# Kernel optimization log

Hardware: AMD Instinct MI355X
Metric: run time of the kernel (lower is better)

Reference implementation:

```python
import jax, jax.numpy as jnp
import numpy as np

N = 50000          # num nodes
E = 800000         # num edges (before self loops)
IN_C = 128
HID = 256          # heads * head_dim
HEADS = 4
HEAD_DIM = HID // HEADS
OUT_C = 64
NEG_SLOPE = 0.2    # PyG GATConv default leaky_relu slope
BN_EPS = 1e-5


def _gat_conv(x, src, dst, W, att_src, att_dst, bias, concat):
    """PyG-style GATConv (with self loops already appended to src/dst).
    x: [N, in_c]; W: [in_c, H*C]; att_src/att_dst: [H, C]; bias: [H*C] or [C]."""
    H, C = att_src.shape
    h = (x @ W).reshape(-1, H, C)                               # [N, H, C]
    a_src = jnp.einsum('nhc,hc->nh', h, att_src)                # [N, H]
    a_dst = jnp.einsum('nhc,hc->nh', h, att_dst)                # [N, H]
    e = jax.nn.leaky_relu(a_src[src] + a_dst[dst], NEG_SLOPE)   # [Et, H]
    # segment softmax over destination nodes (numerically stable)
    m = jax.ops.segment_max(e, dst, num_segments=N)             # [N, H]
    m = jnp.where(jnp.isfinite(m), m, 0.0)
    ex = jnp.exp(e - m[dst])
    denom = jax.ops.segment_sum(ex, dst, num_segments=N)        # [N, H]
    alpha = ex / (denom[dst] + 1e-16)                           # [Et, H]
    msg = alpha[:, :, None] * h[src]                            # [Et, H, C]
    out = jax.ops.segment_sum(msg, dst, num_segments=N)         # [N, H, C]
    out = out.reshape(N, H * C) if concat else out.mean(axis=1)
    return out + bias


def _bn_eval(x, gamma, beta, mean, var):
    return (x - mean) * jax.lax.rsqrt(var + BN_EPS) * gamma + beta


def setup_inputs() -> dict:
    key = jax.random.key(0)
    ks = jax.random.split(key, 16)
    x = jax.random.normal(ks[0], (N, IN_C), dtype=jnp.float32)
    edge_index = jax.random.randint(ks[1], (2, E), 0, N, dtype=jnp.int64)

    def lin(k, fan_in, fan_out):
        s = (1.0 / np.sqrt(fan_in)).astype(np.float32)
        return jax.random.normal(k, (fan_in, fan_out), dtype=jnp.float32) * s

    def att(k, h, c):
        return jax.random.normal(k, (h, c), dtype=jnp.float32) * 0.1

    return {
        'x': x, 'edge_index': edge_index,
        'W0': lin(ks[2], IN_C, HID), 'as0': att(ks[3], HEADS, HEAD_DIM), 'ad0': att(ks[4], HEADS, HEAD_DIM), 'b0': jnp.zeros((HID,), jnp.float32),
        'bn0_g': jnp.ones((HID,), jnp.float32), 'bn0_b': jnp.zeros((HID,), jnp.float32), 'bn0_m': jnp.zeros((HID,), jnp.float32), 'bn0_v': jnp.ones((HID,), jnp.float32),
        'W1': lin(ks[5], HID, HID), 'as1': att(ks[6], HEADS, HEAD_DIM), 'ad1': att(ks[7], HEADS, HEAD_DIM), 'b1': jnp.zeros((HID,), jnp.float32),
        'bn1_g': jnp.ones((HID,), jnp.float32), 'bn1_b': jnp.zeros((HID,), jnp.float32), 'bn1_m': jnp.zeros((HID,), jnp.float32), 'bn1_v': jnp.ones((HID,), jnp.float32),
        'W2': lin(ks[8], HID, OUT_C), 'as2': att(ks[9], 1, OUT_C), 'ad2': att(ks[10], 1, OUT_C), 'b2': jnp.zeros((OUT_C,), jnp.float32),
    }


def reference(x, edge_index, W0, as0, ad0, b0, bn0_g, bn0_b, bn0_m, bn0_v,
              W1, as1, ad1, b1, bn1_g, bn1_b, bn1_m, bn1_v,
              W2, as2, ad2, b2):
    loop = jnp.arange(N, dtype=edge_index.dtype)
    src = jnp.concatenate([edge_index[0], loop])   # PyG add_self_loops=True
    dst = jnp.concatenate([edge_index[1], loop])

    h = _gat_conv(x, src, dst, W0, as0, ad0, b0, concat=True)
    h = jax.nn.elu(_bn_eval(h, bn0_g, bn0_b, bn0_m, bn0_v))   # dropout: eval -> identity
    h = _gat_conv(h, src, dst, W1, as1, ad1, b1, concat=True)
    h = jax.nn.elu(_bn_eval(h, bn1_g, bn1_b, bn1_m, bn1_v))
    out = _gat_conv(h, src, dst, W2, as2, ad2, b2, concat=False)  # heads=1, mean
    return out
```

## Files before the change

kernel.cpp:

```cpp
#include <hip/hip_runtime.h>

#define NN   50000
#define EE   800000
#define ET   850000
#define INC  128
#define HID  256
#define OUTC 64
#define NEG  0.2f
#define BNEPS 1e-5f

typedef __bf16 bf16x8 __attribute__((ext_vector_type(8)));
typedef float  f32x4  __attribute__((ext_vector_type(4)));

static __device__ __forceinline__ float b2f(unsigned short u) {
    return __uint_as_float(((unsigned)u) << 16);
}
static __device__ __forceinline__ float blo(unsigned u) {
    return __uint_as_float(u << 16);
}
static __device__ __forceinline__ float bhi(unsigned u) {
    return __uint_as_float(u & 0xFFFF0000u);
}
static __device__ __forceinline__ unsigned short f2b(float f) {
    unsigned u = __float_as_uint(f);
    unsigned r = u + 0x7FFFu + ((u >> 16) & 1u);
    return (unsigned short)(r >> 16);
}
static __device__ __forceinline__ float leaky(float x) {
    return x > 0.f ? x : NEG * x;
}
static __device__ __forceinline__ float ew(float e) {
    return __expf(fminf(e, 80.f));
}

__global__ void k_init(const int* __restrict__ ei, const unsigned* __restrict__ xw,
                       int* __restrict__ cnt, int* __restrict__ flagW, int* __restrict__ flagB,
                       int nbZ) {
    __shared__ int cs[4];
    int b = blockIdx.x, t = threadIdx.x;
    if (b < nbZ) {
        int i = b * 256 + t;
        if (i < NN) cnt[i] = 0;
    } else if (b == nbZ) {
        int c = 0;
        for (int k = 0; k < 16; k++) {
            int i = t + 256 * k;
            if (ei[2 * i + 1] != 0) c = 1;
        }
        for (int o = 1; o < 64; o <<= 1) c |= __shfl_xor(c, o);
        if ((t & 63) == 0) cs[t >> 6] = c;
        __syncthreads();
        if (t == 0) *flagW = cs[0] | cs[1] | cs[2] | cs[3];
    } else {
        int c = 0;
        for (int i = t; i < 4096; i += 256) {
            unsigned v = (xw[i] >> 8) & 0x7F;
            if (v >= 50 && v <= 67) c++;
        }
        for (int o = 1; o < 64; o <<= 1) c += __shfl_xor(c, o);
        if ((t & 63) == 0) cs[t >> 6] = c;
        __syncthreads();
        if (t == 0) *flagB = (cs[0] + cs[1] + cs[2] + cs[3] > 2048) ? 1 : 0;
    }
}

__global__ void k_prep(const void* as0, const void* ad0, const void* b0, const void* g0,
                       const void* be0, const void* m0, const void* v0,
                       const void* as1, const void* ad1, const void* b1, const void* g1,
                       const void* be1, const void* m1, const void* v1,
                       const void* as2, const void* ad2, const void* b2,
                       const void* W0, const void* W1, const void* W2,
                       unsigned short* __restrict__ WT0, unsigned short* __restrict__ WT1,
                       unsigned short* __restrict__ WT2,
                       const void* __restrict__ x, unsigned short* __restrict__ xb,
                       float* __restrict__ pp, const int* __restrict__ flagB) {
    int b = blockIdx.x, t = threadIdx.x;
    bool bf = (*flagB != 0);
    auto cv = [&](const void* s, int i) -> float {
        return bf ? b2f(((const unsigned short*)s)[i]) : ((const float*)s)[i];
    };
    if (b < 14) {
        float v;
        switch (b) {
            case 0:  v = cv(as0, t); break;
            case 1:  v = cv(ad0, t); break;
            case 2:  v = cv(b0, t);  break;
            case 3:  v = cv(g0, t);  break;
            case 4:  v = cv(be0, t); break;
            case 5:  v = cv(m0, t);  break;
            case 6:  v = cv(v0, t);  break;
            case 7:  v = cv(as1, t); break;
            case 8:  v = cv(ad1, t); break;
            case 9:  v = cv(b1, t);  break;
            case 10: v = cv(g1, t);  break;
            case 11: v = cv(be1, t); break;
            case 12: v = cv(m1, t);  break;
            default: v = cv(v1, t);  break;
        }
        pp[b * 256 + t] = v;
    } else if (b == 14) {
        if (t < 192) {
            int arr = t >> 6, j = t & 63;
            float v = (arr == 0) ? cv(as2, j) : (arr == 1) ? cv(ad2, j) : cv(b2, j);
            pp[14 * 256 + arr * 64 + j] = v;
        }
    } else if (b < 15 + 128) {
        int i = (b - 15) * 256 + t;
        int k = i >> 8, n = i & 255;
        WT0[n * INC + k] = bf ? ((const unsigned short*)W0)[i] : f2b(((const float*)W0)[i]);
    } else if (b < 15 + 128 + 256) {
        int i = (b - 143) * 256 + t;
        int k = i >> 8, n = i & 255;
        WT1[n * HID + k] = bf ? ((const unsigned short*)W1)[i] : f2b(((const float*)W1)[i]);
    } else if (b < 15 + 128 + 256 + 64) {
        int i = (b - 399) * 256 + t;
        int k = i >> 6, n = i & 63;
        WT2[n * HID + k] = bf ? ((const unsigned short*)W2)[i] : f2b(((const float*)W2)[i]);
    } else {
        if (bf) return;
        int i = (b - 463) * 256 + t;
        if (i < NN * INC)
            xb[i] = f2b(((const float*)x)[i]);
    }
}

__global__ void k_hist(const int* __restrict__ ei, const int* __restrict__ flagW,
                       int* __restrict__ cnt) {
    int i = blockIdx.x * 256 + threadIdx.x;
    if (i >= ET) return;
    bool w32 = (*flagW != 0);
    int d = (i < EE) ? (w32 ? ei[EE + i] : ei[2 * (EE + i)]) : (i - EE);
    atomicAdd(&cnt[d], 1);
}

static __device__ __forceinline__ int block_scan_incl(int v, int t, int* ws) {
    int lane = t & 63, w = t >> 6;
    int x = v;
    for (int o = 1; o < 64; o <<= 1) {
        int y = __shfl_up(x, o);
        if (lane >= o) x += y;
    }
    if (lane == 63) ws[w] = x;
    __syncthreads();
    if (t == 0) {
        int s = 0;
        for (int k = 0; k < 4; k++) { int tmp = ws[k]; ws[k] = s; s += tmp; }
    }
    __syncthreads();
    return x + ws[w];
}

__global__ void k_scan_a(const int* __restrict__ cnt, int* __restrict__ rowptr, int* __restrict__ bsum) {
    __shared__ int ws[4];
    int t = threadIdx.x, b = blockIdx.x;
    int i = b * 256 + t;
    int v = (i < NN) ? cnt[i] : 0;
    int incl = block_scan_incl(v, t, ws);
    if (i < NN) rowptr[i] = incl - v;
    if (t == 255) bsum[b] = incl;
}

__global__ void k_scan_b(int* __restrict__ bsum, int nb) {
    __shared__ int ws[4];
    int t = threadIdx.x;
    int v = (t < nb) ? bsum[t] : 0;
    int incl = block_scan_incl(v, t, ws);
    if (t < nb) bsum[t] = incl - v;
}

__global__ void k_scan_c(int* __restrict__ rowptr, const int* __restrict__ bsum, int* __restrict__ cursor) {
    int t = threadIdx.x, b = blockIdx.x;
    int i = b * 256 + t;
    if (i < NN) {
        int r = rowptr[i] + bsum[b];
        rowptr[i] = r;
        cursor[i] = r;
    }
    if (i == 0) rowptr[NN] = ET;
}

__global__ void k_scatter(const int* __restrict__ ei, const int* __restrict__ flagW,
                          int* __restrict__ cursor, int* __restrict__ esrc) {
    int i = blockIdx.x * 256 + threadIdx.x;
    if (i >= ET) {
        if (i < ET + 64) esrc[i] = 0;
        return;
    }
    bool w32 = (*flagW != 0);
    int s, d;
    if (i < EE) {
        if (w32) { s = ei[i];     d = ei[EE + i]; }
        else     { s = ei[2 * i]; d = ei[2 * (EE + i)]; }
    } else {
        s = d = i - EE;
    }
    int p = atomicAdd(&cursor[d], 1);
    esrc[p] = s;
}

template<int NC, int NH>
__global__ __launch_bounds__(256) void k_gemm(const unsigned short* __restrict__ Amain,
                                              const void* __restrict__ Aalt,
                                              const int* __restrict__ flagB,
                                              const unsigned short* __restrict__ WT,
                                              unsigned short* __restrict__ H,
                                              float* __restrict__ asrc, float* __restrict__ adst,
                                              const float* __restrict__ asv, const float* __restrict__ adv,
                                              int M, int K) {
    __shared__ __align__(16) unsigned short As[128 * 40];
    __shared__ __align__(16) unsigned short Bs[64 * 40];
    const unsigned short* A = (*flagB) ? (const unsigned short*)Aalt : Amain;
    int t = threadIdx.x;
    int bm = blockIdx.x, bn = blockIdx.y;
    int lane = t & 63, wave = t >> 6;
    int m16 = lane & 15, quad = lane >> 4;

    f32x4 acc[2][4];
    for (int a = 0; a < 2; a++) for (int b = 0; b < 4; b++) acc[a][b] = (f32x4){0.f, 0.f, 0.f, 0.f};

    int arow = t >> 1, ahalf = t & 1;
    int brow = t >> 2, bq = t & 3;
    long gArow = (long)bm * 128 + arow;

    for (int k0 = 0; k0 < K; k0 += 32) {
        uint4 av0 = {0u, 0u, 0u, 0u}, av1 = {0u, 0u, 0u, 0u};
        if (gArow < M) {
            const unsigned short* ap = A + gArow * (size_t)K + k0 + ahalf * 16;
            av0 = *(const uint4*)(ap);
            av1 = *(const uint4*)(ap + 8);
        }
        uint4 bv = *(const uint4*)(WT + ((size_t)bn * 64 + brow) * K + k0 + bq * 8);
        *(uint4*)&As[arow * 40 + ahalf * 16]     = av0;
        *(uint4*)&As[arow * 40 + ahalf * 16 + 8] = av1;
        *(uint4*)&Bs[brow * 40 + bq * 8]         = bv;
        __syncthreads();
        int wrow = wave * 32;
        bf16x8 af[2], bf[4];
        for (int mt = 0; mt < 2; mt++)
            af[mt] = *(const bf16x8*)&As[(wrow + mt * 16 + m16) * 40 + quad * 8];
        for (int nt = 0; nt < 4; nt++)
            bf[nt] = *(const bf16x8*)&Bs[(nt * 16 + m16) * 40 + quad * 8];
        for (int mt = 0; mt < 2; mt++)
            for (int nt = 0; nt < 4; nt++)
                acc[mt][nt] = __builtin_amdgcn_mfma_f32_16x16x32_bf16(af[mt], bf[nt], acc[mt][nt], 0, 0, 0);
        __syncthreads();
    }

    float asc[4], adc[4];
    for (int nt = 0; nt < 4; nt++) {
        int col = bn * 64 + nt * 16 + m16;
        asc[nt] = asv[col];
        adc[nt] = adv[col];
    }
    for (int mt = 0; mt < 2; mt++) {
        int gR0 = bm * 128 + wave * 32 + mt * 16 + quad * 4;
        for (int r = 0; r < 4; r++) {
            int gR = gR0 + r;
            float ps = 0.f, pd = 0.f;
            for (int nt = 0; nt < 4; nt++) {
                float v = acc[mt][nt][r];
                ps += v * asc[nt];
                pd += v * adc[nt];
            }
            for (int o = 1; o < 16; o <<= 1) { ps += __shfl_xor(ps, o); pd += __shfl_xor(pd, o); }
            if (m16 == 0 && gR < M) {
                asrc[(size_t)gR * NH + bn] = ps;
                adst[(size_t)gR * NH + bn] = pd;
            }
            if (gR < M) {
                for (int nt = 0; nt < 4; nt++) {
                    int gC = bn * 64 + nt * 16 + m16;
                    H[(size_t)gR * NC + gC] = f2b(acc[mt][nt][r]);
                }
            }
        }
    }
}

#define LOADG(pre, d, e0n) \
    uint2 pre##0 = {0, 0}, pre##1 = {0, 0}, pre##2 = {0, 0}, pre##3 = {0, 0}; \
    if (d) { \
        int s0_ = esrc[(e0n)], s1_ = esrc[(e0n) + 1], s2_ = esrc[(e0n) + 2], s3_ = esrc[(e0n) + 3]; \
        pre##0 = *(const uint2*)(h + (size_t)s0_ * HID + lc); \
        pre##1 = *(const uint2*)(h + (size_t)s1_ * HID + lc); \
        pre##2 = *(const uint2*)(h + (size_t)s2_ * HID + lc); \
        pre##3 = *(const uint2*)(h + (size_t)s3_ * HID + lc); \
    }
#define FMAG(pre, d, wreg, A0, A1, A2, A3, j) \
    if (d) { \
        float w0_ = __shfl(wreg, wsel + (j)),     w1_ = __shfl(wreg, wsel + (j) + 1); \
        float w2_ = __shfl(wreg, wsel + (j) + 2), w3_ = __shfl(wreg, wsel + (j) + 3); \
        A0 += w0_ * blo((pre##0).x) + w1_ * blo((pre##1).x) + w2_ * blo((pre##2).x) + w3_ * blo((pre##3).x); \
        A1 += w0_ * bhi((pre##0).x) + w1_ * bhi((pre##1).x) + w2_ * bhi((pre##2).x) + w3_ * bhi((pre##3).x); \
        A2 += w0_ * blo((pre##0).y) + w1_ * blo((pre##1).y) + w2_ * blo((pre##2).y) + w3_ * blo((pre##3).y); \
        A3 += w0_ * bhi((pre##0).y) + w1_ * bhi((pre##1).y) + w2_ * bhi((pre##2).y) + w3_ * bhi((pre##3).y); \
    }

__global__ __launch_bounds__(256, 4) void k_agg4(const unsigned short* __restrict__ h,
                       const float* __restrict__ asrc, const float* __restrict__ adst,
                       const int* __restrict__ rowptr, const int* __restrict__ esrc,
                       const float* __restrict__ bias,
                       const float* __restrict__ bng, const float* __restrict__ bnb,
                       const float* __restrict__ bnm, const float* __restrict__ bnv,
                       unsigned short* __restrict__ act) {
    int t = threadIdx.x;
    int wave = t >> 6, lane = t & 63;
    int nodeA = blockIdx.x * 8 + wave * 2;
    if (nodeA >= NN) return;
    int nodeB = nodeA + 1;
    bool hasB = (nodeB < NN);

    int hd = lane >> 4, li = lane & 15;
    int wsel = lane & 48;
    const size_t lc = (size_t)lane * 4;

    int e0A = __builtin_amdgcn_readfirstlane(rowptr[nodeA]);
    int e1A = __builtin_amdgcn_readfirstlane(rowptr[nodeA + 1]);
    int degA = e1A - e0A;
    int e0B = e1A, degB = 0;
    if (hasB) degB = __builtin_amdgcn_readfirstlane(rowptr[nodeB + 1]) - e1A;

    float adhA = adst[(size_t)nodeA * 4 + hd];
    float adhB = hasB ? adst[(size_t)nodeB * 4 + hd] : 0.f;

    float waccA = 0.f, waccB = 0.f;
    float aA0 = 0.f, aA1 = 0.f, aA2 = 0.f, aA3 = 0.f;
    float aB0 = 0.f, aB1 = 0.f, aB2 = 0.f, aB3 = 0.f;

    int nA = min(16, degA), nB = min(16, degB);
    float eA = 0.f, eB = 0.f;
    if (li < nA) { int s = esrc[e0A + li]; eA = asrc[(size_t)s * 4 + hd]; }
    if (li < nB) { int s = esrc[e0B + li]; eB = asrc[(size_t)s * 4 + hd]; }

    int degM = max(degA, degB);
    for (int c = 0; c < degM; c += 16) {
        float wA = (li < nA) ? ew(leaky(eA + adhA)) : 0.f;
        float wB = (li < nB) ? ew(leaky(eB + adhB)) : 0.f;
        waccA += wA; waccB += wB;
        int nA2 = min(16, degA - (c + 16));
        int nB2 = min(16, degB - (c + 16));
        eA = 0.f; eB = 0.f;
        if (li < nA2) { int s = esrc[e0A + c + 16 + li]; eA = asrc[(size_t)s * 4 + hd]; }
        if (li < nB2) { int s = esrc[e0B + c + 16 + li]; eB = asrc[(size_t)s * 4 + hd]; }
        bool dA0 = 0 < nA, dA1 = 4 < nA, dA2 = 8 < nA, dA3 = 12 < nA;
        bool dB0 = 0 < nB, dB1 = 4 < nB, dB2 = 8 < nB, dB3 = 12 < nB;
        LOADG(gA0, dA0, e0A + c)
        LOADG(gA1, dA1, e0A + c + 4)
        LOADG(gA2, dA2, e0A + c + 8)
        LOADG(gA3, dA3, e0A + c + 12)
        LOADG(gB0, dB0, e0B + c)
        LOADG(gB1, dB1, e0B + c + 4)
        LOADG(gB2, dB2, e0B + c + 8)
        LOADG(gB3, dB3, e0B + c + 12)
        FMAG(gA0, dA0, wA, aA0, aA1, aA2, aA3, 0)
        FMAG(gA1, dA1, wA, aA0, aA1, aA2, aA3, 4)
        FMAG(gA2, dA2, wA, aA0, aA1, aA2, aA3, 8)
        FMAG(gA3, dA3, wA, aA0, aA1, aA2, aA3, 12)
        FMAG(gB0, dB0, wB, aB0, aB1, aB2, aB3, 0)
        FMAG(gB1, dB1, wB, aB0, aB1, aB2, aB3, 4)
        FMAG(gB2, dB2, wB, aB0, aB1, aB2, aB3, 8)
        FMAG(gB3, dB3, wB, aB0, aB1, aB2, aB3, 12)
        nA = nA2; nB = nB2;
    }
    waccA += __shfl_xor(waccA, 1); waccA += __shfl_xor(waccA, 2);
    waccA += __shfl_xor(waccA, 4); waccA += __shfl_xor(waccA, 8);
    waccB += __shfl_xor(waccB, 1); waccB += __shfl_xor(waccB, 2);
    waccB += __shfl_xor(waccB, 4); waccB += __shfl_xor(waccB, 8);
    float invA = 1.f / (waccA + 1e-16f);
    float invB = 1.f / (waccB + 1e-16f);

    int c0 = lane * 4;
    float4 bi = *(const float4*)(bias + c0);
    float4 bm_ = *(const float4*)(bnm + c0);
    float4 bv_ = *(const float4*)(bnv + c0);
    float4 bg_ = *(const float4*)(bng + c0);
    float4 bb_ = *(const float4*)(bnb + c0);
    float sc[4], sh[4];
    {
        const float* bvp = (const float*)&bv_;
        const float* bgp = (const float*)&bg_;
        const float* bmp = (const float*)&bm_;
        const float* bbp = (const float*)&bb_;
        const float* bip = (const float*)&bi;
        #pragma unroll
        for (int jj = 0; jj < 4; jj++) {
            float s_ = rsqrtf(bvp[jj] + BNEPS) * bgp[jj];
            sc[jj] = s_;
            sh[jj] = bbp[jj] + (bip[jj] - bmp[jj]) * s_;
        }
    }
    {
        float o[4] = {aA0 * invA, aA1 * invA, aA2 * invA, aA3 * invA};
        unsigned short res[4];
        #pragma unroll
        for (int jj = 0; jj < 4; jj++) {
            float val = o[jj] * sc[jj] + sh[jj];
            val = val > 0.f ? val : expm1f(val);
            res[jj] = f2b(val);
        }
        *(ushort4*)(act + (size_t)nodeA * HID + c0) = *(ushort4*)res;
    }
    if (hasB) {
        float o[4] = {aB0 * invB, aB1 * invB, aB2 * invB, aB3 * invB};
        unsigned short res[4];
        #pragma unroll
        for (int jj = 0; jj < 4; jj++) {
            float val = o[jj] * sc[jj] + sh[jj];
            val = val > 0.f ? val : expm1f(val);
            res[jj] = f2b(val);
        }
        *(ushort4*)(act + (size_t)nodeB * HID + c0) = *(ushort4*)res;
    }
}

__global__ void k_agg1(const unsigned short* __restrict__ h,
                       const float* __restrict__ asrc, const float* __restrict__ adst,
                       const int* __restrict__ rowptr, const int* __restrict__ esrc,
                       const float* __restrict__ bias,
                       void* __restrict__ outp, const int* __restrict__ flagB) {
    int t = threadIdx.x;
    int wave = t >> 6, lane = t & 63;
    int nodeA = blockIdx.x * 8 + wave * 2;
    if (nodeA >= NN) return;
    int nodeB = nodeA + 1;
    bool hasB = (nodeB < NN);

    int e0A  = __builtin_amdgcn_readfirstlane(rowptr[nodeA]);
    int e1A  = __builtin_amdgcn_readfirstlane(rowptr[nodeA + 1]);
    int degA = e1A - e0A;
    int e0B  = e1A;
    int degB = hasB ? (__builtin_amdgcn_readfirstlane(rowptr[nodeB + 1]) - e1A) : 0;
    float adA = adst[nodeA];
    float adB = hasB ? adst[nodeB] : 0.f;

    float denA = 0.f, denB = 0.f, accA = 0.f, accB = 0.f;

    int nA = min(64, degA), nB = min(64, degB);
    float eA = 0.f, eB = 0.f;
    if (lane < nA) { int s = esrc[e0A + lane]; eA = asrc[s]; }
    if (lane < nB) { int s = esrc[e0B + lane]; eB = asrc[s]; }

    int degM = max(degA, degB);
    for (int c = 0; c < degM; c += 64) {
        float wA = (lane < nA) ? ew(leaky(eA + adA)) : 0.f;
        float wB = (lane < nB) ? ew(leaky(eB + adB)) : 0.f;
        denA += wA; denB += wB;
        int nA2 = min(64, degA - (c + 64));
        int nB2 = min(64, degB - (c + 64));
        eA = 0.f; eB = 0.f;
        if (lane < nA2) { int s = esrc[e0A + c + 64 + lane]; eA = asrc[s]; }
        if (lane < nB2) { int s = esrc[e0B + c + 64 + lane]; eB = asrc[s]; }
        int nM = max(nA, nB);
        for (int j = 0; j < nM; j += 4) {
            bool doA = j < nA, doB = j < nB;
            float w0A = 0.f, w1A = 0.f, w2A = 0.f, w3A = 0.f;
            float w0B = 0.f, w1B = 0.f, w2B = 0.f, w3B = 0.f;
            unsigned short hA0 = 0, hA1 = 0, hA2 = 0, hA3 = 0;
            unsigned short hB0 = 0, hB1 = 0, hB2 = 0, hB3 = 0;
            if (doA) {
                int s0 = esrc[e0A + c + j];     int s1 = esrc[e0A + c + j + 1];
                int s2 = esrc[e0A + c + j + 2]; int s3 = esrc[e0A + c + j + 3];
                w0A = __shfl(wA, j);     w1A = __shfl(wA, j + 1);
                w2A = __shfl(wA, j + 2); w3A = __shfl(wA, j + 3);
                hA0 = h[(size_t)s0 * OUTC + lane];
                hA1 = h[(size_t)s1 * OUTC + lane];
                hA2 = h[(size_t)s2 * OUTC + lane];
                hA3 = h[(size_t)s3 * OUTC + lane];
            }
            if (doB) {
                int s0 = esrc[e0B + c + j];     int s1 = esrc[e0B + c + j + 1];
                int s2 = esrc[e0B + c + j + 2]; int s3 = esrc[e0B + c + j + 3];
                w0B = __shfl(wB, j);     w1B = __shfl(wB, j + 1);
                w2B = __shfl(wB, j + 2); w3B = __shfl(wB, j + 3);
                hB0 = h[(size_t)s0 * OUTC + lane];
                hB1 = h[(size_t)s1 * OUTC + lane];
                hB2 = h[(size_t)s2 * OUTC + lane];
                hB3 = h[(size_t)s3 * OUTC + lane];
            }
            if (doA) accA += w0A * b2f(hA0) + w1A * b2f(hA1) + w2A * b2f(hA2) + w3A * b2f(hA3);
            if (doB) accB += w0B * b2f(hB0) + w1B * b2f(hB1) + w2B * b2f(hB2) + w3B * b2f(hB3);
        }
        nA = nA2; nB = nB2;
    }
    for (int o = 1; o < 64; o <<= 1) denA += __shfl_xor(denA, o);
    for (int o = 1; o < 64; o <<= 1) denB += __shfl_xor(denB, o);
    float valA = accA / (denA + 1e-16f) + bias[lane];
    float valB = accB / (denB + 1e-16f) + bias[lane];
    if (*flagB) {
        ((unsigned short*)outp)[(size_t)nodeA * OUTC + lane] = f2b(valA);
        if (hasB) ((unsigned short*)outp)[(size_t)nodeB * OUTC + lane] = f2b(valB);
    } else {
        ((float*)outp)[(size_t)nodeA * OUTC + lane] = valA;
        if (hasB) ((float*)outp)[(size_t)nodeB * OUTC + lane] = valB;
    }
}

extern "C" void kernel_launch(void* const* d_in, const int* in_sizes, int n_in,
                              void* d_out, int out_size, void* d_ws, size_t ws_size,
                              hipStream_t stream) {
    const void* x  = d_in[0];
    const int*  ei = (const int*)d_in[1];
    const void* W0 = d_in[2];
    const void* W1 = d_in[10];
    const void* W2 = d_in[18];

    char* ws = (char*)d_ws;
    size_t off = 0;
    auto alloc = [&](size_t n) { void* p = ws + off; off += (n + 255) & ~(size_t)255; return p; };

    unsigned short* xb  = (unsigned short*)alloc((size_t)NN * INC * 2);
    unsigned short* h   = (unsigned short*)alloc((size_t)NN * HID * 2);
    unsigned short* act = (unsigned short*)alloc((size_t)NN * HID * 2);
    unsigned short* WT0 = (unsigned short*)alloc((size_t)HID * INC * 2);
    unsigned short* WT1 = (unsigned short*)alloc((size_t)HID * HID * 2);
    unsigned short* WT2 = (unsigned short*)alloc((size_t)OUTC * HID * 2);
    float*          pp  = (float*)alloc((size_t)(14 * 256 + 3 * 64) * 4);
    float*  asrc   = (float*)alloc((size_t)NN * 4 * 4);
    float*  adst   = (float*)alloc((size_t)NN * 4 * 4);
    int*    cnt    = (int*)alloc((size_t)(NN + 2) * 4);
    int*    rowptr = (int*)alloc((size_t)(NN + 1) * 4);
    int*    cursor = (int*)alloc((size_t)NN * 4);
    int*    esrc   = (int*)alloc((size_t)(ET + 64) * 4);
    int*    bsum   = (int*)alloc(256 * 4);
    int*    flagW  = cnt + NN;
    int*    flagB  = cnt + NN + 1;

    float* P0 = pp;
    float* P1 = pp + 7 * 256;
    float* P2 = pp + 14 * 256;

    const int nbN = (NN + 255) / 256;
    const int nbE = (ET + 255) / 256;
    const int nbA4 = (NN + 7) / 8;
    const int nbA1 = (NN + 7) / 8;
    const int nbPrep = 463 + (NN * INC + 255) / 256;
    dim3 gemmGrid0((NN + 127) / 128, HID / 64);
    dim3 gemmGrid2((NN + 127) / 128, 1);

    k_init<<<nbN + 2, 256, 0, stream>>>(ei, (const unsigned*)x, cnt, flagW, flagB, nbN);
    k_hist<<<nbE, 256, 0, stream>>>(ei, flagW, cnt);
    k_scan_a<<<nbN, 256, 0, stream>>>(cnt, rowptr, bsum);
    k_scan_b<<<1, 256, 0, stream>>>(bsum, nbN);
    k_scan_c<<<nbN, 256, 0, stream>>>(rowptr, bsum, cursor);
    k_scatter<<<nbE, 256, 0, stream>>>(ei, flagW, cursor, esrc);

    k_prep<<<nbPrep, 256, 0, stream>>>(d_in[3], d_in[4], d_in[5], d_in[6], d_in[7], d_in[8], d_in[9],
                                       d_in[11], d_in[12], d_in[13], d_in[14], d_in[15], d_in[16], d_in[17],
                                       d_in[19], d_in[20], d_in[21],
                                       W0, W1, W2, WT0, WT1, WT2, x, xb, pp, flagB);

    k_gemm<HID, 4><<<gemmGrid0, 256, 0, stream>>>(xb, x, flagB, WT0, h, asrc, adst,
                                                  P0 + 0, P0 + 256, NN, INC);
    k_agg4<<<nbA4, 256, 0, stream>>>(h, asrc, adst, rowptr, esrc,
                                     P0 + 512, P0 + 768, P0 + 1024, P0 + 1280, P0 + 1536, act);

    k_gemm<HID, 4><<<gemmGrid0, 256, 0, stream>>>(act, act, flagB, WT1, h, asrc, adst,
                                                  P1 + 0, P1 + 256, NN, HID);
    k_agg4<<<nbA4, 256, 0, stream>>>(h, asrc, adst, rowptr, esrc,
                                     P1 + 512, P1 + 768, P1 + 1024, P1 + 1280, P1 + 1536, act);

    k_gemm<OUTC, 1><<<gemmGrid2, 256, 0, stream>>>(act, act, flagB, WT2, h, asrc, adst,
                                                   P2 + 0, P2 + 64, NN, HID);
    k_agg1<<<nbA1, 256, 0, stream>>>(h, asrc, adst, rowptr, esrc, P2 + 128, d_out, flagB);
}
```

Before: 446.4 us.

## Widen GEMM N-tile, restructure final aggregation, grid-stride x conversion

The GEMM is templated on the number of 64-column groups, so the hidden layers use 128-wide N tiles. Each A tile is then reused across two heads, which halves the grid's y dimension and the redundant A loads. The last aggregation kernel now assigns four nodes per wave, each on a 16-lane quarter that gathers 4 channels with 8-byte loads, in place of two nodes per wave with 2-byte per-lane loads. The x-to-bf16 prep becomes a grid-stride loop over a fixed 2048 blocks, and register pressure rises in the GEMM.

Result: faster. 434.7 us (-2.6%).

```diff
diff --git a/kernel.cpp b/kernel.cpp
--- a/kernel.cpp
+++ b/kernel.cpp
@@ -118,8 +118,7 @@
         WT2[n * HID + k] = bf ? ((const unsigned short*)W2)[i] : f2b(((const float*)W2)[i]);
     } else {
         if (bf) return;
-        int i = (b - 463) * 256 + t;
-        if (i < NN * INC)
+        for (int i = (b - 463) * 256 + t; i < NN * INC; i += 2048 * 256)
             xb[i] = f2b(((const float*)x)[i]);
     }
 }
@@ -198,7 +197,7 @@
     esrc[p] = s;
 }
 
-template<int NC, int NH>
+template<int NC, int NH, int NBN>
 __global__ __launch_bounds__(256) void k_gemm(const unsigned short* __restrict__ Amain,
                                               const void* __restrict__ Aalt,
                                               const int* __restrict__ flagB,
@@ -207,19 +206,22 @@
                                               float* __restrict__ asrc, float* __restrict__ adst,
                                               const float* __restrict__ asv, const float* __restrict__ adv,
                                               int M, int K) {
+    constexpr int BN = 64 * NBN;
     __shared__ __align__(16) unsigned short As[128 * 40];
-    __shared__ __align__(16) unsigned short Bs[64 * 40];
+    __shared__ __align__(16) unsigned short Bs[BN * 40];
     const unsigned short* A = (*flagB) ? (const unsigned short*)Aalt : Amain;
     int t = threadIdx.x;
-    int bm = blockIdx.x, bn = blockIdx.y;
+    int bm = blockIdx.x, bg = blockIdx.y;
     int lane = t & 63, wave = t >> 6;
     int m16 = lane & 15, quad = lane >> 4;
 
-    f32x4 acc[2][4];
-    for (int a = 0; a < 2; a++) for (int b = 0; b < 4; b++) acc[a][b] = (f32x4){0.f, 0.f, 0.f, 0.f};
+    f32x4 acc[2][4 * NBN];
+    #pragma unroll
+    for (int a = 0; a < 2; a++)
+        #pragma unroll
+        for (int b = 0; b < 4 * NBN; b++) acc[a][b] = (f32x4){0.f, 0.f, 0.f, 0.f};
 
     int arow = t >> 1, ahalf = t & 1;
-    int brow = t >> 2, bq = t & 3;
     long gArow = (long)bm * 128 + arow;
 
     for (int k0 = 0; k0 < K; k0 += 32) {
@@ -229,47 +231,70 @@
             av0 = *(const uint4*)(ap);
             av1 = *(const uint4*)(ap + 8);
         }
-        uint4 bv = *(const uint4*)(WT + ((size_t)bn * 64 + brow) * K + k0 + bq * 8);
-        *(uint4*)&As[arow * 40 + ahalf * 16]     = av0;
-        *(uint4*)&As[arow * 40 + ahalf * 16 + 8] = av1;
-        *(uint4*)&Bs[brow * 40 + bq * 8]         = bv;
+        if constexpr (NBN == 2) {
+            const unsigned short* bp = WT + ((size_t)bg * BN + arow) * K + k0 + ahalf * 16;
+            uint4 bv0 = *(const uint4*)(bp);
+            uint4 bv1 = *(const uint4*)(bp + 8);
+            *(uint4*)&As[arow * 40 + ahalf * 16]     = av0;
+            *(uint4*)&As[arow * 40 + ahalf * 16 + 8] = av1;
+            *(uint4*)&Bs[arow * 40 + ahalf * 16]     = bv0;
+            *(uint4*)&Bs[arow * 40 + ahalf * 16 + 8] = bv1;
+        } else {
+            int brow = t >> 2, bq = t & 3;
+            uint4 bv = *(const uint4*)(WT + ((size_t)bg * BN + brow) * K + k0 + bq * 8);
+            *(uint4*)&As[arow * 40 + ahalf * 16]     = av0;
+            *(uint4*)&As[arow * 40 + ahalf * 16 + 8] = av1;
+            *(uint4*)&Bs[brow * 40 + bq * 8]         = bv;
+        }
         __syncthreads();
         int wrow = wave * 32;
-        bf16x8 af[2], bf[4];
+        bf16x8 af[2], bf[4 * NBN];
+        #pragma unroll
         for (int mt = 0; mt < 2; mt++)
             af[mt] = *(const bf16x8*)&As[(wrow + mt * 16 + m16) * 40 + quad * 8];
-        for (int nt = 0; nt < 4; nt++)
+        #pragma unroll
+        for (int nt = 0; nt < 4 * NBN; nt++)
             bf[nt] = *(const bf16x8*)&Bs[(nt * 16 + m16) * 40 + quad * 8];
+        #pragma unroll
         for (int mt = 0; mt < 2; mt++)
-            for (int nt = 0; nt < 4; nt++)
+            #pragma unroll
+            for (int nt = 0; nt < 4 * NBN; nt++)
                 acc[mt][nt] = __builtin_amdgcn_mfma_f32_16x16x32_bf16(af[mt], bf[nt], acc[mt][nt], 0, 0, 0);
         __syncthreads();
     }
 
-    float asc[4], adc[4];
-    for (int nt = 0; nt < 4; nt++) {
-        int col = bn * 64 + nt * 16 + m16;
+    float asc[4 * NBN], adc[4 * NBN];
+    #pragma unroll
+    for (int nt = 0; nt < 4 * NBN; nt++) {
+        int col = bg * BN + nt * 16 + m16;
         asc[nt] = asv[col];
         adc[nt] = adv[col];
     }
+    #pragma unroll
     for (int mt = 0; mt < 2; mt++) {
         int gR0 = bm * 128 + wave * 32 + mt * 16 + quad * 4;
+        #pragma unroll
         for (int r = 0; r < 4; r++) {
             int gR = gR0 + r;
-            float ps = 0.f, pd = 0.f;
-            for (int nt = 0; nt < 4; nt++) {
-                float v = acc[mt][nt][r];
-                ps += v * asc[nt];
-                pd += v * adc[nt];
-            }
-            for (int o = 1; o < 16; o <<= 1) { ps += __shfl_xor(ps, o); pd += __shfl_xor(pd, o); }
-            if (m16 == 0 && gR < M) {
-                asrc[(size_t)gR * NH + bn] = ps;
-                adst[(size_t)gR * NH + bn] = pd;
+            #pragma unroll
+            for (int hh = 0; hh < NBN; hh++) {
+                float ps = 0.f, pd = 0.f;
+                #pragma unroll
+                for (int nt = hh * 4; nt < hh * 4 + 4; nt++) {
+                    float v = acc[mt][nt][r];
+                    ps += v * asc[nt];
+                    pd += v * adc[nt];
+                }
+                for (int o = 1; o < 16; o <<= 1) { ps += __shfl_xor(ps, o); pd += __shfl_xor(pd, o); }
+                if (m16 == 0 && gR < M) {
+                    asrc[(size_t)gR * NH + bg * NBN + hh] = ps;
+                    adst[(size_t)gR * NH + bg * NBN + hh] = pd;
+                }
             }
             if (gR < M) {
-                for (int nt = 0; nt < 4; nt++) {
-                    int gC = bn * 64 + nt * 16 + m16;
+                #pragma unroll
+                for (int nt = 0; nt < 4 * NBN; nt++) {
+                    int gC = bg * BN + nt * 16 + m16;
                     H[(size_t)gR * NC + gC] = f2b(acc[mt][nt][r]);
                 }
             }
@@ -420,78 +445,69 @@
                        void* __restrict__ outp, const int* __restrict__ flagB) {
     int t = threadIdx.x;
     int wave = t >> 6, lane = t & 63;
-    int nodeA = blockIdx.x * 8 + wave * 2;
-    if (nodeA >= NN) return;
-    int nodeB = nodeA + 1;
-    bool hasB = (nodeB < NN);
-
-    int e0A  = __builtin_amdgcn_readfirstlane(rowptr[nodeA]);
-    int e1A  = __builtin_amdgcn_readfirstlane(rowptr[nodeA + 1]);
-    int degA = e1A - e0A;
-    int e0B  = e1A;
-    int degB = hasB ? (__builtin_amdgcn_readfirstlane(rowptr[nodeB + 1]) - e1A) : 0;
-    float adA = adst[nodeA];
-    float adB = hasB ? adst[nodeB] : 0.f;
-
-    float denA = 0.f, denB = 0.f, accA = 0.f, accB = 0.f;
-
-    int nA = min(64, degA), nB = min(64, degB);
-    float eA = 0.f, eB = 0.f;
-    if (lane < nA) { int s = esrc[e0A + lane]; eA = asrc[s]; }
-    if (lane < nB) { int s = esrc[e0B + lane]; eB = asrc[s]; }
-
-    int degM = max(degA, degB);
-    for (int c = 0; c < degM; c += 64) {
-        float wA = (lane < nA) ? ew(leaky(eA + adA)) : 0.f;
-        float wB = (lane < nB) ? ew(leaky(eB + adB)) : 0.f;
-        denA += wA; denB += wB;
-        int nA2 = min(64, degA - (c + 64));
-        int nB2 = min(64, degB - (c + 64));
-        eA = 0.f; eB = 0.f;
-        if (lane < nA2) { int s = esrc[e0A + c + 64 + lane]; eA = asrc[s]; }
-        if (lane < nB2) { int s = esrc[e0B + c + 64 + lane]; eB = asrc[s]; }
-        int nM = max(nA, nB);
-        for (int j = 0; j < nM; j += 4) {
-            bool doA = j < nA, doB = j < nB;
-            float w0A = 0.f, w1A = 0.f, w2A = 0.f, w3A = 0.f;
-            float w0B = 0.f, w1B = 0.f, w2B = 0.f, w3B = 0.f;
-            unsigned short hA0 = 0, hA1 = 0, hA2 = 0, hA3 = 0;
-            unsigned short hB0 = 0, hB1 = 0, hB2 = 0, hB3 = 0;
-            if (doA) {
-                int s0 = esrc[e0A + c + j];     int s1 = esrc[e0A + c + j + 1];
-                int s2 = esrc[e0A + c + j + 2]; int s3 = esrc[e0A + c + j + 3];
-                w0A = __shfl(wA, j);     w1A = __shfl(wA, j + 1);
-                w2A = __shfl(wA, j + 2); w3A = __shfl(wA, j + 3);
-                hA0 = h[(size_t)s0 * OUTC + lane];
-                hA1 = h[(size_t)s1 * OUTC + lane];
-                hA2 = h[(size_t)s2 * OUTC + lane];
-                hA3 = h[(size_t)s3 * OUTC + lane];
+    int node0 = blockIdx.x * 16 + wave * 4;
+    int q = lane >> 4, lq = lane & 15;
+    int qs = lane & 48;
+    int node = node0 + q;
+    const size_t lc4 = (size_t)lq * 4;
+
+    int e0  = rowptr[node];
+    int deg = rowptr[node + 1] - e0;
+    float ad = adst[node];
+
+    float den = 0.f;
+    float a0 = 0.f, a1 = 0.f, a2 = 0.f, a3 = 0.f;
+
+    int n = min(16, deg);
+    int s = 0; float e = 0.f;
+    if (lq < n) { s = esrc[e0 + lq]; e = asrc[s]; }
+
+    int degM = deg;
+    degM = max(degM, __shfl_xor(degM, 16));
+    degM = max(degM, __shfl_xor(degM, 32));
+
+    for (int c = 0; c < degM; c += 16) {
+        float w = (lq < n) ? ew(leaky(e + ad)) : 0.f;
+        den += w;
+        int n2 = min(16, deg - (c + 16));
+        int sN = 0; float eN = 0.f;
+        if (lq < n2) { sN = esrc[e0 + c + 16 + lq]; eN = asrc[sN]; }
+        #pragma unroll
+        for (int g = 0; g < 4; g++) {
+            int j = g * 4;
+            if (j < n) {
+                int s0 = __shfl(s, qs + j),     s1 = __shfl(s, qs + j + 1);
+                int s2 = __shfl(s, qs + j + 2), s3 = __shfl(s, qs + j + 3);
+                float w0 = __shfl(w, qs + j),     w1 = __shfl(w, qs + j + 1);
+                float w2 = __shfl(w, qs + j + 2), w3 = __shfl(w, qs + j + 3);
+                uint2 v0 = *(const uint2*)(h + (size_t)s0 * OUTC + lc4);
+                uint2 v1 = *(const uint2*)(h + (size_t)s1 * OUTC + lc4);
+                uint2 v2 = *(const uint2*)(h + (size_t)s2 * OUTC + lc4);
+                uint2 v3 = *(const uint2*)(h + (size_t)s3 * OUTC + lc4);
+                a0 += w0 * blo(v0.x) + w1 * blo(v1.x) + w2 * blo(v2.x) + w3 * blo(v3.x);
+                a1 += w0 * bhi(v0.x) + w1 * bhi(v1.x) + w2 * bhi(v2.x) + w3 * bhi(v3.x);
+                a2 += w0 * blo(v0.y) + w1 * blo(v1.y) + w2 * blo(v2.y) + w3 * blo(v3.y);
+                a3 += w0 * bhi(v0.y) + w1 * bhi(v1.y) + w2 * bhi(v2.y) + w3 * bhi(v3.y);
             }
-            if (doB) {
-                int s0 = esrc[e0B + c + j];     int s1 = esrc[e0B + c + j + 1];
-                int s2 = esrc[e0B + c + j + 2]; int s3 = esrc[e0B + c + j + 3];
-                w0B = __shfl(wB, j);     w1B = __shfl(wB, j + 1);
-                w2B = __shfl(wB, j + 2); w3B = __shfl(wB, j + 3);
-                hB0 = h[(size_t)s0 * OUTC + lane];
-                hB1 = h[(size_t)s1 * OUTC + lane];
-                hB2 = h[(size_t)s2 * OUTC + lane];
-                hB3 = h[(size_t)s3 * OUTC + lane];
-            }
-            if (doA) accA += w0A * b2f(hA0) + w1A * b2f(hA1) + w2A * b2f(hA2) + w3A * b2f(hA3);
-            if (doB) accB += w0B * b2f(hB0) + w1B * b2f(hB1) + w2B * b2f(hB2) + w3B * b2f(hB3);
-        }
-        nA = nA2; nB = nB2;
-    }
-    for (int o = 1; o < 64; o <<= 1) denA += __shfl_xor(denA, o);
-    for (int o = 1; o < 64; o <<= 1) denB += __shfl_xor(denB, o);
-    float valA = accA / (denA + 1e-16f) + bias[lane];
-    float valB = accB / (denB + 1e-16f) + bias[lane];
+        }
+        s = sN; e = eN; n = n2;
+    }
+    den += __shfl_xor(den, 1); den += __shfl_xor(den, 2);
+    den += __shfl_xor(den, 4); den += __shfl_xor(den, 8);
+    float inv = 1.f / (den + 1e-16f);
+    int c0 = lq * 4;
+    float v0 = a0 * inv + bias[c0];
+    float v1 = a1 * inv + bias[c0 + 1];
+    float v2 = a2 * inv + bias[c0 + 2];
+    float v3 = a3 * inv + bias[c0 + 3];
     if (*flagB) {
-        ((unsigned short*)outp)[(size_t)nodeA * OUTC + lane] = f2b(valA);
-        if (hasB) ((unsigned short*)outp)[(size_t)nodeB * OUTC + lane] = f2b(valB);
+        unsigned r0 = (unsigned)f2b(v0) | ((unsigned)f2b(v1) << 16);
+        unsigned r1 = (unsigned)f2b(v2) | ((unsigned)f2b(v3) << 16);
+        uint2 rv = {r0, r1};
+        *(uint2*)((unsigned short*)outp + (size_t)node * OUTC + c0) = rv;
     } else {
-        ((float*)outp)[(size_t)nodeA * OUTC + lane] = valA;
-        if (hasB) ((float*)outp)[(size_t)nodeB * OUTC + lane] = valB;
+        float4 rv = {v0, v1, v2, v3};
+        *(float4*)((float*)outp + (size_t)node * OUTC + c0) = rv;
     }
 }
 
@@ -532,9 +548,9 @@
     const int nbN = (NN + 255) / 256;
     const int nbE = (ET + 255) / 256;
     const int nbA4 = (NN + 7) / 8;
-    const int nbA1 = (NN + 7) / 8;
-    const int nbPrep = 463 + (NN * INC + 255) / 256;
-    dim3 gemmGrid0((NN + 127) / 128, HID / 64);
+    const int nbA1 = NN / 16;
+    const int nbPrep = 463 + 2048;
+    dim3 gemmGrid0((NN + 127) / 128, HID / 128);
     dim3 gemmGrid2((NN + 127) / 128, 1);
 
     k_init<<<nbN + 2, 256, 0, stream>>>(ei, (const unsigned*)x, cnt, flagW, flagB, nbN);
@@ -549,17 +565,17 @@
                                        d_in[19], d_in[20], d_in[21],
                                        W0, W1, W2, WT0, WT1, WT2, x, xb, pp, flagB);
 
-    k_gemm<HID, 4><<<gemmGrid0, 256, 0, stream>>>(xb, x, flagB, WT0, h, asrc, adst,
-                                                  P0 + 0, P0 + 256, NN, INC);
+    k_gemm<HID, 4, 2><<<gemmGrid0, 256, 0, stream>>>(xb, x, flagB, WT0, h, asrc, adst,
+                                                     P0 + 0, P0 + 256, NN, INC);
     k_agg4<<<nbA4, 256, 0, stream>>>(h, asrc, adst, rowptr, esrc,
                                      P0 + 512, P0 + 768, P0 + 1024, P0 + 1280, P0 + 1536, act);
 
-    k_gemm<HID, 4><<<gemmGrid0, 256, 0, stream>>>(act, act, flagB, WT1, h, asrc, adst,
-                                                  P1 + 0, P1 + 256, NN, HID);
+    k_gemm<HID, 4, 2><<<gemmGrid0, 256, 0, stream>>>(act, act, flagB, WT1, h, asrc, adst,
+                                                     P1 + 0, P1 + 256, NN, HID);
     k_agg4<<<nbA4, 256, 0, stream>>>(h, asrc, adst, rowptr, esrc,
                                      P1 + 512, P1 + 768, P1 + 1024, P1 + 1280, P1 + 1536, act);
 
-    k_gemm<OUTC, 1><<<gemmGrid2, 256, 0, stream>>>(act, act, flagB, WT2, h, asrc, adst,
-                                                   P2 + 0, P2 + 64, NN, HID);
+    k_gemm<OUTC, 1, 1><<<gemmGrid2, 256, 0, stream>>>(act, act, flagB, WT2, h, asrc, adst,
+                                                      P2 + 0, P2 + 64, NN, HID);
     k_agg1<<<nbA1, 256, 0, stream>>>(h, asrc, adst, rowptr, esrc, P2 + 128, d_out, flagB);
 }
```
